# Optimization experiments

Hardware: AMD Instinct MI355X
Metric: run time of the kernel (lower is better)

The kernel has to match this reference:

```python
import jax, jax.numpy as jnp
import numpy as np

EPS = 1e-12
TOPK = 6

def _l2norm(x):
    # matches torch F.normalize(p=2, eps=1e-12)
    n = jnp.linalg.norm(x, axis=-1, keepdims=True)
    return x / jnp.maximum(n, EPS)

def setup_inputs() -> dict:
    key = jax.random.key(0)
    k1, k2 = jax.random.split(key)
    nC, M, P, d = 5, 512, 196, 384
    support = jax.random.normal(k1, (nC, P, d), dtype=jnp.float32)
    query = jax.random.normal(k2, (M, P, d), dtype=jnp.float32)
    scale_cls = jnp.full((1,), 10.0, dtype=jnp.float32)  # init value in module
    bias = jnp.zeros((1,), dtype=jnp.float32)
    return {"support": support, "query": query, "scale_cls": scale_cls, "bias": bias}

def reference(support, query, scale_cls, bias):
    q = _l2norm(query)      # [M, P, d]
    s = _l2norm(support)    # [nC, P, d]
    # batched cosine similarity between every query patch and support patch
    sim = jnp.einsum('mpd,cqd->mcpq', q, s)   # [M, nC, P, P]
    # max over support patches, then sum of top-6 query-patch matches
    m = sim.max(axis=3)                        # [M, nC, P]
    top6 = jax.lax.top_k(m, TOPK)[0].sum(axis=-1)  # [M, nC]
    cls_scores = top6[None]                    # [1, M, nC] (unsqueeze(0))
    return scale_cls * (cls_scores + bias)
```

## Files before the change

kernel.cpp:

```cpp
#include <hip/hip_runtime.h>
#include <hip/hip_bf16.h>
#include <cstdint>

typedef __attribute__((ext_vector_type(8))) short short8;
typedef __attribute__((ext_vector_type(4))) float floatx4;

#define NC   5
#define PP   196
#define DD   384
#define MM   512
#define ROWS (MM * PP)
#define NRB  3136
#define BR   32
#define EPSN 1e-12f

#define NTILES      16
#define TILE_BYTES  49152
#define KSTEP_BYTES 4096

__device__ __forceinline__ unsigned enc_f(float f) {
    unsigned u = __float_as_uint(f);
    return (u & 0x80000000u) ? ~u : (u | 0x80000000u);
}
__device__ __forceinline__ float dec_f(unsigned u) {
    unsigned b = (u & 0x80000000u) ? (u ^ 0x80000000u) : ~u;
    return __uint_as_float(b);
}
#define ENC_NEG_INF 0x007FFFFFu

__device__ __forceinline__ int cls_of(int col) {
    return (col >= 784) ? 4 : (col >= 588) ? 3 : (col >= 392) ? 2 : (col >= 196) ? 1 : 0;
}

__global__ __launch_bounds__(256) void k_norm0(const float* __restrict__ sup,
                                               float* __restrict__ sinv) {
    int wid = threadIdx.x >> 6, lane = threadIdx.x & 63;
    int r = blockIdx.x * 4 + wid;
    if (r >= NC * PP) return;
    const float* src = sup + (size_t)r * DD;
    float s = 0.f;
    #pragma unroll
    for (int j = 0; j < 6; ++j) { float v = src[lane + j * 64]; s += v * v; }
    #pragma unroll
    for (int off = 1; off < 64; off <<= 1) s += __shfl_xor(s, off, 64);
    if (lane == 0) sinv[r] = 1.0f / fmaxf(sqrtf(s), EPSN);
}

__global__ __launch_bounds__(256) void k_swz(const float* __restrict__ sup,
                                             const float* __restrict__ sinv,
                                             __hip_bfloat16* __restrict__ snw) {
    int s = blockIdx.x * 256 + threadIdx.x;
    int lane = s & 63;
    int r1 = s >> 6;
    int ct = r1 & 3;
    int r2 = r1 >> 2;
    int kk = r2 % 12;
    int t  = r2 / 12;
    int c16 = lane & 15, quad = lane >> 4;
    int col = t * 64 + ct * 16 + c16;
    if (col > NC * PP - 1) col = NC * PP - 1;
    int srow = col;
    const float* sp = sup + (size_t)srow * DD + kk * 32 + quad * 8;
    float inv = sinv[srow];
    alignas(16) __hip_bfloat16 hb[8];
    #pragma unroll
    for (int e = 0; e < 8; ++e) hb[e] = __float2bfloat16(sp[e] * inv);
    *(uint4*)((char*)snw + (size_t)s * 16) = *(const uint4*)hb;
}

__global__ __launch_bounds__(256, 4) void k_gemm_max(const float* __restrict__ q,
                                                     const __hip_bfloat16* __restrict__ snw,
                                                     float* __restrict__ rowmaxg) {
    __shared__ __hip_bfloat16 As[12 * 2 * 64 * 8];
    __shared__ unsigned rmax[BR * NC];
    __shared__ float rss[BR];

    const int tid  = threadIdx.x;
    const int row0 = blockIdx.x * BR;
    const int lane = tid & 63;
    const int wav  = tid >> 6;

    for (int i = tid; i < BR * NC; i += 256) rmax[i] = ENC_NEG_INF;

    {
        const int arow = tid >> 3;
        const int asub = tid & 7;
        const int rt   = arow >> 4, c16 = arow & 15;
        const float* src = q + (size_t)(row0 + arow) * DD;
        float ss = 0.f;
        #pragma unroll
        for (int i = 0; i < 6; ++i) {
            int ch = asub + i * 8;
            const floatx4* p = (const floatx4*)(src + ch * 8);
            floatx4 x0 = __builtin_nontemporal_load(p);
            floatx4 x1 = __builtin_nontemporal_load(p + 1);
            ss += x0.x*x0.x + x0.y*x0.y + x0.z*x0.z + x0.w*x0.w
                + x1.x*x1.x + x1.y*x1.y + x1.z*x1.z + x1.w*x1.w;
            alignas(16) __hip_bfloat16 hb[8];
            hb[0] = __float2bfloat16(x0.x); hb[1] = __float2bfloat16(x0.y);
            hb[2] = __float2bfloat16(x0.z); hb[3] = __float2bfloat16(x0.w);
            hb[4] = __float2bfloat16(x1.x); hb[5] = __float2bfloat16(x1.y);
            hb[6] = __float2bfloat16(x1.z); hb[7] = __float2bfloat16(x1.w);
            int kk = ch >> 2, quad = ch & 3;
            *(uint4*)&As[((kk * 2 + rt) * 64 + quad * 16 + c16) * 8] = *(const uint4*)hb;
        }
        ss += __shfl_xor(ss, 1, 64);
        ss += __shfl_xor(ss, 2, 64);
        ss += __shfl_xor(ss, 4, 64);
        if (asub == 0) rss[arow] = ss;
    }

    const char* bbase = (const char*)snw + (size_t)wav * TILE_BYTES + (size_t)lane * 16;
    short8 b0[4], b1[4], b2[4], a[2];
    #pragma unroll
    for (int ct = 0; ct < 4; ++ct) b0[ct] = ((const short8*)(bbase + 0 * KSTEP_BYTES))[ct * 64];
    #pragma unroll
    for (int ct = 0; ct < 4; ++ct) b1[ct] = ((const short8*)(bbase + 1 * KSTEP_BYTES))[ct * 64];
    #pragma unroll
    for (int ct = 0; ct < 4; ++ct) b2[ct] = ((const short8*)(bbase + 2 * KSTEP_BYTES))[ct * 64];

    __syncthreads();

    #define LOAD_NEXT(buf, step)                                                     \
        do {                                                                         \
            int nk = kk + 3 + (step);                                                \
            if (nk < 12) {                                                           \
                _Pragma("unroll")                                                    \
                for (int ct = 0; ct < 4; ++ct)                                       \
                    buf[ct] = ((const short8*)(bbase + nk * KSTEP_BYTES))[ct * 64];  \
            } else if (g + 4 < NTILES) {                                             \
                _Pragma("unroll")                                                    \
                for (int ct = 0; ct < 4; ++ct)                                       \
                    buf[ct] = ((const short8*)(bbase + 4 * TILE_BYTES +              \
                                               (nk - 12) * KSTEP_BYTES))[ct * 64];   \
            }                                                                        \
        } while (0)

    #define MFMA_STEP(buf, kkoff)                                                    \
        do {                                                                         \
            _Pragma("unroll")                                                        \
            for (int rt = 0; rt < 2; ++rt)                                           \
                a[rt] = *(const short8*)&As[(((kk + (kkoff)) * 2 + rt) * 64 + lane) * 8]; \
            _Pragma("unroll")                                                        \
            for (int ct = 0; ct < 4; ++ct)                                           \
                _Pragma("unroll")                                                    \
                for (int rt = 0; rt < 2; ++rt)                                       \
                    acc[ct][rt] = __builtin_amdgcn_mfma_f32_16x16x32_bf16(           \
                        buf[ct], a[rt], acc[ct][rt], 0, 0, 0);                       \
        } while (0)

    #pragma unroll 1
    for (int g = wav; g < NTILES; g += 4) {
        floatx4 acc[4][2];
        #pragma unroll
        for (int i = 0; i < 4; ++i)
            #pragma unroll
            for (int j = 0; j < 2; ++j) acc[i][j] = (floatx4){0.f, 0.f, 0.f, 0.f};

        #pragma unroll 1
        for (int kk = 0; kk < 12; kk += 3) {
            MFMA_STEP(b0, 0); LOAD_NEXT(b0, 0);
            MFMA_STEP(b1, 1); LOAD_NEXT(b1, 1);
            MFMA_STEP(b2, 2); LOAD_NEXT(b2, 2);
        }

        {
            const int colbase = g * 64;
            int ce = colbase + 63; if (ce > NC * PP - 1) ce = NC * PP - 1;
            const int clo = cls_of(colbase), chi = cls_of(ce);
            const int quad = lane >> 4;
            if (clo == chi) {
                #pragma unroll
                for (int rt = 0; rt < 2; ++rt) {
                    float mx = acc[0][rt][0];
                    #pragma unroll
                    for (int ct = 0; ct < 4; ++ct)
                        #pragma unroll
                        for (int reg = 0; reg < 4; ++reg)
                            if (ct | reg) mx = fmaxf(mx, acc[ct][rt][reg]);
                    mx = fmaxf(mx, __shfl_xor(mx, 16, 64));
                    mx = fmaxf(mx, __shfl_xor(mx, 32, 64));
                    if (lane < 16) atomicMax(&rmax[(rt * 16 + lane) * NC + clo], enc_f(mx));
                }
            } else {
                const int bnd = chi * PP;
                #pragma unroll
                for (int rt = 0; rt < 2; ++rt) {
                    float mlo = -INFINITY, mhi = -INFINITY;
                    #pragma unroll
                    for (int ct = 0; ct < 4; ++ct)
                        #pragma unroll
                        for (int reg = 0; reg < 4; ++reg) {
                            int scol = colbase + ct * 16 + quad * 4 + reg;
                            if (scol >= bnd) mhi = fmaxf(mhi, acc[ct][rt][reg]);
                            else             mlo = fmaxf(mlo, acc[ct][rt][reg]);
                        }
                    mlo = fmaxf(mlo, __shfl_xor(mlo, 16, 64));
                    mlo = fmaxf(mlo, __shfl_xor(mlo, 32, 64));
                    mhi = fmaxf(mhi, __shfl_xor(mhi, 16, 64));
                    mhi = fmaxf(mhi, __shfl_xor(mhi, 32, 64));
                    if (lane < 16) {
                        atomicMax(&rmax[(rt * 16 + lane) * NC + clo], enc_f(mlo));
                        atomicMax(&rmax[(rt * 16 + lane) * NC + chi], enc_f(mhi));
                    }
                }
            }
        }
        bbase += 4 * TILE_BYTES;
    }

    __syncthreads();
    for (int i = tid; i < BR * NC; i += 256) {
        int c = i >> 5, row = i & 31;
        float inv = 1.0f / fmaxf(sqrtf(rss[row]), EPSN);
        __builtin_nontemporal_store(dec_f(rmax[row * NC + c]) * inv,
                                    &rowmaxg[(size_t)c * ROWS + row0 + row]);
    }
}

__global__ __launch_bounds__(256) void k_top6(const float* __restrict__ rowmaxg,
                                              const float* __restrict__ scale,
                                              const float* __restrict__ bias,
                                              float* __restrict__ out) {
    int wav = threadIdx.x >> 6, lane = threadIdx.x & 63;
    int pair = blockIdx.x * 4 + wav;
    if (pair >= MM * NC) return;
    int m = pair / NC, c = pair % NC;
    size_t base = (size_t)c * ROWS + (size_t)m * PP;
    float v[4];
    #pragma unroll
    for (int i = 0; i < 4; ++i) {
        int p = lane + i * 64;
        v[i] = (p < PP) ? rowmaxg[base + p] : -INFINITY;
    }
    float sum = 0.f;
    for (int t = 0; t < 6; ++t) {
        float bv = v[0]; int bi = 0;
        #pragma unroll
        for (int i = 1; i < 4; ++i) { if (v[i] > bv) { bv = v[i]; bi = i; } }
        int gid = bi * 64 + lane;
        #pragma unroll
        for (int off = 1; off < 64; off <<= 1) {
            float ov = __shfl_xor(bv, off, 64);
            int og  = __shfl_xor(gid, off, 64);
            if (ov > bv || (ov == bv && og < gid)) { bv = ov; gid = og; }
        }
        sum += bv;
        if ((gid & 63) == lane) v[gid >> 6] = -INFINITY;
    }
    if (lane == 0) out[pair] = scale[0] * (sum + bias[0]);
}

extern "C" void kernel_launch(void* const* d_in, const int* in_sizes, int n_in,
                              void* d_out, int out_size, void* d_ws, size_t ws_size,
                              hipStream_t stream) {
    const float* support = (const float*)d_in[0];
    const float* query   = (const float*)d_in[1];
    const float* scale   = (const float*)d_in[2];
    const float* bias    = (const float*)d_in[3];
    float* out = (float*)d_out;

    char* ws = (char*)d_ws;
    __hip_bfloat16* snw = (__hip_bfloat16*)ws;
    float* sinv         = (float*)(ws + 786432);
    float* rowmaxg      = (float*)(ws + 786432 + 4096);

    hipLaunchKernelGGL(k_norm0,   dim3(245),  dim3(256), 0, stream, support, sinv);
    hipLaunchKernelGGL(k_swz,     dim3(192),  dim3(256), 0, stream, support, sinv, snw);
    hipLaunchKernelGGL(k_gemm_max,dim3(NRB),  dim3(256), 0, stream, query, snw, rowmaxg);
    hipLaunchKernelGGL(k_top6,    dim3(640),  dim3(256), 0, stream, rowmaxg, scale, bias, out);
}
```

Before: 304.5 us.

## Double row tile to 64 query rows per block with software-pipelined A/B fetch

Each block now processes 64 query rows instead of 32. Every wave therefore issues 4x4 MFMA tiles per B fragment, which halves how often the support matrix is re-read from L2 per query row. The k-loop is fully unrolled with double-buffered A fragments from LDS and rotating B register buffers that prefetch across tile boundaries. Occupancy drops to 2 blocks per CU because accumulator registers and LDS use both double, which may reduce latency hiding.

Result: slower. 377.3 us (+23.9%).

```diff
diff --git a/kernel.cpp b/kernel.cpp
--- a/kernel.cpp
+++ b/kernel.cpp
@@ -10,8 +10,8 @@
 #define DD   384
 #define MM   512
 #define ROWS (MM * PP)
-#define NRB  3136
-#define BR   32
+#define NRB  1568
+#define BR   64
 #define EPSN 1e-12f
 
 #define NTILES      16
@@ -68,10 +68,10 @@
     *(uint4*)((char*)snw + (size_t)s * 16) = *(const uint4*)hb;
 }
 
-__global__ __launch_bounds__(256, 4) void k_gemm_max(const float* __restrict__ q,
+__global__ __launch_bounds__(256, 2) void k_gemm_max(const float* __restrict__ q,
                                                      const __hip_bfloat16* __restrict__ snw,
                                                      float* __restrict__ rowmaxg) {
-    __shared__ __hip_bfloat16 As[12 * 2 * 64 * 8];
+    __shared__ __hip_bfloat16 As[12 * 4 * 64 * 8];
     __shared__ unsigned rmax[BR * NC];
     __shared__ float rss[BR];
 
@@ -83,15 +83,14 @@
     for (int i = tid; i < BR * NC; i += 256) rmax[i] = ENC_NEG_INF;
 
     {
-        const int arow = tid >> 3;
-        const int asub = tid & 7;
-        const int rt   = arow >> 4, c16 = arow & 15;
-        const float* src = q + (size_t)(row0 + arow) * DD;
+        const int c16  = lane & 15;
+        const int quad = lane >> 4;
+        const int arow = wav * 16 + c16;
+        const float* src = q + (size_t)(row0 + arow) * DD + quad * 8;
         float ss = 0.f;
         #pragma unroll
-        for (int i = 0; i < 6; ++i) {
-            int ch = asub + i * 8;
-            const floatx4* p = (const floatx4*)(src + ch * 8);
+        for (int i = 0; i < 12; ++i) {
+            const floatx4* p = (const floatx4*)(src + i * 32);
             floatx4 x0 = __builtin_nontemporal_load(p);
             floatx4 x1 = __builtin_nontemporal_load(p + 1);
             ss += x0.x*x0.x + x0.y*x0.y + x0.z*x0.z + x0.w*x0.w
@@ -101,68 +100,77 @@
             hb[2] = __float2bfloat16(x0.z); hb[3] = __float2bfloat16(x0.w);
             hb[4] = __float2bfloat16(x1.x); hb[5] = __float2bfloat16(x1.y);
             hb[6] = __float2bfloat16(x1.z); hb[7] = __float2bfloat16(x1.w);
-            int kk = ch >> 2, quad = ch & 3;
-            *(uint4*)&As[((kk * 2 + rt) * 64 + quad * 16 + c16) * 8] = *(const uint4*)hb;
+            *(uint4*)&As[((i * 4 + wav) * 64 + lane) * 8] = *(const uint4*)hb;
         }
-        ss += __shfl_xor(ss, 1, 64);
-        ss += __shfl_xor(ss, 2, 64);
-        ss += __shfl_xor(ss, 4, 64);
-        if (asub == 0) rss[arow] = ss;
+        ss += __shfl_xor(ss, 16, 64);
+        ss += __shfl_xor(ss, 32, 64);
+        if (quad == 0) rss[arow] = ss;
     }
 
     const char* bbase = (const char*)snw + (size_t)wav * TILE_BYTES + (size_t)lane * 16;
-    short8 b0[4], b1[4], b2[4], a[2];
-    #pragma unroll
-    for (int ct = 0; ct < 4; ++ct) b0[ct] = ((const short8*)(bbase + 0 * KSTEP_BYTES))[ct * 64];
-    #pragma unroll
-    for (int ct = 0; ct < 4; ++ct) b1[ct] = ((const short8*)(bbase + 1 * KSTEP_BYTES))[ct * 64];
-    #pragma unroll
-    for (int ct = 0; ct < 4; ++ct) b2[ct] = ((const short8*)(bbase + 2 * KSTEP_BYTES))[ct * 64];
-
-    __syncthreads();
-
-    #define LOAD_NEXT(buf, step)                                                     \
-        do {                                                                         \
-            int nk = kk + 3 + (step);                                                \
-            if (nk < 12) {                                                           \
-                _Pragma("unroll")                                                    \
-                for (int ct = 0; ct < 4; ++ct)                                       \
-                    buf[ct] = ((const short8*)(bbase + nk * KSTEP_BYTES))[ct * 64];  \
-            } else if (g + 4 < NTILES) {                                             \
-                _Pragma("unroll")                                                    \
-                for (int ct = 0; ct < 4; ++ct)                                       \
-                    buf[ct] = ((const short8*)(bbase + 4 * TILE_BYTES +              \
-                                               (nk - 12) * KSTEP_BYTES))[ct * 64];   \
-            }                                                                        \
-        } while (0)
-
-    #define MFMA_STEP(buf, kkoff)                                                    \
-        do {                                                                         \
-            _Pragma("unroll")                                                        \
-            for (int rt = 0; rt < 2; ++rt)                                           \
-                a[rt] = *(const short8*)&As[(((kk + (kkoff)) * 2 + rt) * 64 + lane) * 8]; \
+    short8 b0[4], b1[4], b2[4], a[2][4];
+
+    #define BFETCH(buf, nk)                                                          \
+        do { const char* p_ = bbase + (nk) * KSTEP_BYTES;                            \
             _Pragma("unroll")                                                        \
             for (int ct = 0; ct < 4; ++ct)                                           \
+                buf[ct] = *(const short8*)(p_ + ct * 1024);                          \
+        } while (0)
+
+    #define BFETCHX(buf, nkx)                                                        \
+        do { if (g + 4 < NTILES) {                                                   \
+            const char* p_ = bbase + 4 * TILE_BYTES + (nkx) * KSTEP_BYTES;           \
+            _Pragma("unroll")                                                        \
+            for (int ct = 0; ct < 4; ++ct)                                           \
+                buf[ct] = *(const short8*)(p_ + ct * 1024);                          \
+        } } while (0)
+
+    #define AFETCH(pre, kkn)                                                         \
+        do { _Pragma("unroll")                                                       \
+            for (int rt = 0; rt < 4; ++rt)                                           \
+                a[pre][rt] = *(const short8*)&As[(((kkn) * 4 + rt) * 64 + lane) * 8];\
+        } while (0)
+
+    #define MFMAS(use, buf)                                                          \
+        do { _Pragma("unroll")                                                       \
+            for (int ct = 0; ct < 4; ++ct)                                           \
                 _Pragma("unroll")                                                    \
-                for (int rt = 0; rt < 2; ++rt)                                       \
+                for (int rt = 0; rt < 4; ++rt)                                       \
                     acc[ct][rt] = __builtin_amdgcn_mfma_f32_16x16x32_bf16(           \
-                        buf[ct], a[rt], acc[ct][rt], 0, 0, 0);                       \
+                        buf[ct], a[use][rt], acc[ct][rt], 0, 0, 0);                  \
         } while (0)
+
+    #define STEP(use, pre, kpre, buf, nk)   do { AFETCH(pre, kpre); MFMAS(use, buf); BFETCH(buf, nk);   } while (0)
+    #define STEPX(use, pre, kpre, buf, nkx) do { AFETCH(pre, kpre); MFMAS(use, buf); BFETCHX(buf, nkx); } while (0)
+
+    BFETCH(b0, 0);
+    BFETCH(b1, 1);
+    BFETCH(b2, 2);
+
+    __syncthreads();
+
+    AFETCH(0, 0);
 
     #pragma unroll 1
     for (int g = wav; g < NTILES; g += 4) {
-        floatx4 acc[4][2];
+        floatx4 acc[4][4];
         #pragma unroll
         for (int i = 0; i < 4; ++i)
             #pragma unroll
-            for (int j = 0; j < 2; ++j) acc[i][j] = (floatx4){0.f, 0.f, 0.f, 0.f};
-
-        #pragma unroll 1
-        for (int kk = 0; kk < 12; kk += 3) {
-            MFMA_STEP(b0, 0); LOAD_NEXT(b0, 0);
-            MFMA_STEP(b1, 1); LOAD_NEXT(b1, 1);
-            MFMA_STEP(b2, 2); LOAD_NEXT(b2, 2);
-        }
+            for (int j = 0; j < 4; ++j) acc[i][j] = (floatx4){0.f, 0.f, 0.f, 0.f};
+
+        STEP (0, 1, 1,  b0, 3);
+        STEP (1, 0, 2,  b1, 4);
+        STEP (0, 1, 3,  b2, 5);
+        STEP (1, 0, 4,  b0, 6);
+        STEP (0, 1, 5,  b1, 7);
+        STEP (1, 0, 6,  b2, 8);
+        STEP (0, 1, 7,  b0, 9);
+        STEP (1, 0, 8,  b1, 10);
+        STEP (0, 1, 9,  b2, 11);
+        STEPX(1, 0, 10, b0, 0);
+        STEPX(0, 1, 11, b1, 1);
+        STEPX(1, 0, 0,  b2, 2);
 
         {
             const int colbase = g * 64;
@@ -171,7 +179,7 @@
             const int quad = lane >> 4;
             if (clo == chi) {
                 #pragma unroll
-                for (int rt = 0; rt < 2; ++rt) {
+                for (int rt = 0; rt < 4; ++rt) {
                     float mx = acc[0][rt][0];
                     #pragma unroll
                     for (int ct = 0; ct < 4; ++ct)
@@ -185,7 +193,7 @@
             } else {
                 const int bnd = chi * PP;
                 #pragma unroll
-                for (int rt = 0; rt < 2; ++rt) {
+                for (int rt = 0; rt < 4; ++rt) {
                     float mlo = -INFINITY, mhi = -INFINITY;
                     #pragma unroll
                     for (int ct = 0; ct < 4; ++ct)
@@ -211,7 +219,7 @@
 
     __syncthreads();
     for (int i = tid; i < BR * NC; i += 256) {
-        int c = i >> 5, row = i & 31;
+        int c = i >> 6, row = i & 63;
         float inv = 1.0f / fmaxf(sqrtf(rss[row]), EPSN);
         __builtin_nontemporal_store(dec_f(rmax[row * NC + c]) * inv,
                                     &rowmaxg[(size_t)c * ROWS + row0 + row]);
```

## Double-buffer A fragments in GEMM loop and remap query staging per wave

Applied to the files above, without the earlier changes.

Query staging is remapped so each wave loads one row-tile and one K-half. Each lane now writes its bf16 fragment directly at its own MFMA slot, and the row norm is reduced in two partial sums. The main loop moves from a three-deep B register rotation to a two-deep one, with A fragments from LDS prefetched into a second register set one step ahead of the MFMAs. The aim is to hide LDS latency and lower register pressure. The trade-off is less lookahead on global B loads.

Result: no change. 309.1 us (+1.5%).

```diff
diff --git a/kernel.cpp b/kernel.cpp
--- a/kernel.cpp
+++ b/kernel.cpp
@@ -73,7 +73,7 @@
                                                      float* __restrict__ rowmaxg) {
     __shared__ __hip_bfloat16 As[12 * 2 * 64 * 8];
     __shared__ unsigned rmax[BR * NC];
-    __shared__ float rss[BR];
+    __shared__ float rss[2 * BR];
 
     const int tid  = threadIdx.x;
     const int row0 = blockIdx.x * BR;
@@ -83,15 +83,16 @@
     for (int i = tid; i < BR * NC; i += 256) rmax[i] = ENC_NEG_INF;
 
     {
-        const int arow = tid >> 3;
-        const int asub = tid & 7;
-        const int rt   = arow >> 4, c16 = arow & 15;
-        const float* src = q + (size_t)(row0 + arow) * DD;
+        const int c16  = lane & 15;
+        const int quad = lane >> 4;
+        const int rt   = wav & 1;
+        const int kh   = wav >> 1;
+        const int arow = rt * 16 + c16;
+        const float* src = q + (size_t)(row0 + arow) * DD + kh * 192 + quad * 8;
         float ss = 0.f;
         #pragma unroll
         for (int i = 0; i < 6; ++i) {
-            int ch = asub + i * 8;
-            const floatx4* p = (const floatx4*)(src + ch * 8);
+            const floatx4* p = (const floatx4*)(src + i * 32);
             floatx4 x0 = __builtin_nontemporal_load(p);
             floatx4 x1 = __builtin_nontemporal_load(p + 1);
             ss += x0.x*x0.x + x0.y*x0.y + x0.z*x0.z + x0.w*x0.w
@@ -101,53 +102,61 @@
             hb[2] = __float2bfloat16(x0.z); hb[3] = __float2bfloat16(x0.w);
             hb[4] = __float2bfloat16(x1.x); hb[5] = __float2bfloat16(x1.y);
             hb[6] = __float2bfloat16(x1.z); hb[7] = __float2bfloat16(x1.w);
-            int kk = ch >> 2, quad = ch & 3;
-            *(uint4*)&As[((kk * 2 + rt) * 64 + quad * 16 + c16) * 8] = *(const uint4*)hb;
-        }
-        ss += __shfl_xor(ss, 1, 64);
-        ss += __shfl_xor(ss, 2, 64);
-        ss += __shfl_xor(ss, 4, 64);
-        if (asub == 0) rss[arow] = ss;
+            int kk = kh * 6 + i;
+            *(uint4*)&As[((kk * 2 + rt) * 64 + lane) * 8] = *(const uint4*)hb;
+        }
+        ss += __shfl_xor(ss, 16, 64);
+        ss += __shfl_xor(ss, 32, 64);
+        if (lane < 16) rss[kh * BR + rt * 16 + lane] = ss;
     }
 
     const char* bbase = (const char*)snw + (size_t)wav * TILE_BYTES + (size_t)lane * 16;
-    short8 b0[4], b1[4], b2[4], a[2];
-    #pragma unroll
-    for (int ct = 0; ct < 4; ++ct) b0[ct] = ((const short8*)(bbase + 0 * KSTEP_BYTES))[ct * 64];
-    #pragma unroll
-    for (int ct = 0; ct < 4; ++ct) b1[ct] = ((const short8*)(bbase + 1 * KSTEP_BYTES))[ct * 64];
-    #pragma unroll
-    for (int ct = 0; ct < 4; ++ct) b2[ct] = ((const short8*)(bbase + 2 * KSTEP_BYTES))[ct * 64];
-
-    __syncthreads();
-
-    #define LOAD_NEXT(buf, step)                                                     \
-        do {                                                                         \
-            int nk = kk + 3 + (step);                                                \
-            if (nk < 12) {                                                           \
+    short8 b0[4], b1[4], a[2][2];
+
+    #define BFETCH(buf, nk)                                                          \
+        do { const char* p_ = bbase + (nk) * KSTEP_BYTES;                            \
+            _Pragma("unroll")                                                        \
+            for (int ct = 0; ct < 4; ++ct)                                           \
+                buf[ct] = *(const short8*)(p_ + ct * 1024);                          \
+        } while (0)
+
+    #define BLOADN(buf, nkv)                                                         \
+        do { int nk_ = (nkv);                                                        \
+            if (nk_ < 12) {                                                          \
+                const char* p_ = bbase + nk_ * KSTEP_BYTES;                          \
                 _Pragma("unroll")                                                    \
                 for (int ct = 0; ct < 4; ++ct)                                       \
-                    buf[ct] = ((const short8*)(bbase + nk * KSTEP_BYTES))[ct * 64];  \
+                    buf[ct] = *(const short8*)(p_ + ct * 1024);                      \
             } else if (g + 4 < NTILES) {                                             \
+                const char* p_ = bbase + 4 * TILE_BYTES + (nk_ - 12) * KSTEP_BYTES;  \
                 _Pragma("unroll")                                                    \
                 for (int ct = 0; ct < 4; ++ct)                                       \
-                    buf[ct] = ((const short8*)(bbase + 4 * TILE_BYTES +              \
-                                               (nk - 12) * KSTEP_BYTES))[ct * 64];   \
+                    buf[ct] = *(const short8*)(p_ + ct * 1024);                      \
             }                                                                        \
         } while (0)
 
-    #define MFMA_STEP(buf, kkoff)                                                    \
-        do {                                                                         \
+    #define AFETCH(pre, kkn)                                                         \
+        do { int kn_ = (kkn);                                                        \
             _Pragma("unroll")                                                        \
             for (int rt = 0; rt < 2; ++rt)                                           \
-                a[rt] = *(const short8*)&As[(((kk + (kkoff)) * 2 + rt) * 64 + lane) * 8]; \
-            _Pragma("unroll")                                                        \
+                a[pre][rt] = *(const short8*)&As[((kn_ * 2 + rt) * 64 + lane) * 8];  \
+        } while (0)
+
+    #define MFMAS(use, buf)                                                          \
+        do { _Pragma("unroll")                                                       \
             for (int ct = 0; ct < 4; ++ct)                                           \
                 _Pragma("unroll")                                                    \
                 for (int rt = 0; rt < 2; ++rt)                                       \
                     acc[ct][rt] = __builtin_amdgcn_mfma_f32_16x16x32_bf16(           \
-                        buf[ct], a[rt], acc[ct][rt], 0, 0, 0);                       \
-        } while (0)
+                        buf[ct], a[use][rt], acc[ct][rt], 0, 0, 0);                  \
+        } while (0)
+
+    BFETCH(b0, 0);
+    BFETCH(b1, 1);
+
+    __syncthreads();
+
+    AFETCH(0, 0);
 
     #pragma unroll 1
     for (int g = wav; g < NTILES; g += 4) {
@@ -158,10 +167,13 @@
             for (int j = 0; j < 2; ++j) acc[i][j] = (floatx4){0.f, 0.f, 0.f, 0.f};
 
         #pragma unroll 1
-        for (int kk = 0; kk < 12; kk += 3) {
-            MFMA_STEP(b0, 0); LOAD_NEXT(b0, 0);
-            MFMA_STEP(b1, 1); LOAD_NEXT(b1, 1);
-            MFMA_STEP(b2, 2); LOAD_NEXT(b2, 2);
+        for (int kk = 0; kk < 12; kk += 2) {
+            AFETCH(1, kk + 1);
+            MFMAS(0, b0);
+            BLOADN(b0, kk + 2);
+            AFETCH(0, (kk + 2 < 12) ? (kk + 2) : 0);
+            MFMAS(1, b1);
+            BLOADN(b1, kk + 3);
         }
 
         {
@@ -212,7 +224,7 @@
     __syncthreads();
     for (int i = tid; i < BR * NC; i += 256) {
         int c = i >> 5, row = i & 31;
-        float inv = 1.0f / fmaxf(sqrtf(rss[row]), EPSN);
+        float inv = 1.0f / fmaxf(sqrtf(rss[row] + rss[BR + row]), EPSN);
         __builtin_nontemporal_store(dec_f(rmax[row * NC + c]) * inv,
                                     &rowmaxg[(size_t)c * ROWS + row0 + row]);
     }
```
